# Performance work log

Measured on AMD Instinct MI355X. Metric: run time of the kernel, lower is better.

Reference implementation:

```python
import jax, jax.numpy as jnp
import numpy as np

DIM = 512
L = 4096
B, H, W = 8, 64, 64
EPS = 1e-06
BN_EPS = 1e-05


def setup_inputs() -> dict:
    key = jax.random.key(0)
    ks = jax.random.split(key, 16)
    s = 1.0 / np.sqrt(DIM)
    d = {
        'x': jax.random.normal(ks[0], (B, DIM, H, W), dtype=jnp.float32),
        'pos_emb': jax.random.normal(ks[1], (1, L, DIM), dtype=jnp.float32),
        'Wq': jax.random.uniform(ks[2], (DIM, DIM), jnp.float32, -s, s),
        'bq': jax.random.uniform(ks[3], (DIM,), jnp.float32, -s, s),
        'Wk': jax.random.uniform(ks[4], (DIM, DIM), jnp.float32, -s, s),
        'bk': jax.random.uniform(ks[5], (DIM,), jnp.float32, -s, s),
        'Wv': jax.random.uniform(ks[6], (DIM, DIM), jnp.float32, -s, s),
        'bv': jax.random.uniform(ks[7], (DIM,), jnp.float32, -s, s),
        'Wq1': jax.random.uniform(ks[8], (DIM, DIM), jnp.float32, -s, s),
        'bq1': jax.random.uniform(ks[9], (DIM,), jnp.float32, -s, s),
        'Wk1': jax.random.uniform(ks[10], (DIM, DIM), jnp.float32, -s, s),
        'bk1': jax.random.uniform(ks[11], (DIM,), jnp.float32, -s, s),
        'gamma': jax.random.normal(ks[12], (1,), jnp.float32) * 0.1,
        'bn_weight': jnp.ones((DIM,), jnp.float32),
        'bn_bias': jnp.zeros((DIM,), jnp.float32),
    }
    return d


def reference(x, pos_emb, Wq, bq, Wk, bk, Wv, bv, Wq1, bq1, Wk1, bk1, gamma, bn_weight, bn_bias):
    Bb, C, Hh, Ww = x.shape
    # [B,C,H,W] -> [B, L, C] tokens
    xs = x.transpose(0, 2, 3, 1).reshape(Bb, Hh * Ww, C) + pos_emb
    Q = jax.nn.relu(xs @ Wq.T + bq)   # kernel_fun = ReLU
    K = jax.nn.relu(xs @ Wk.T + bk)
    V = xs @ Wv.T + bv
    Q1 = xs @ Wq1.T + bq1
    K1 = xs @ Wk1.T + bk1
    # torch einsum 'blc,bcc,bl->blc' uses only diag(KV); compute it directly:
    # diagKV[b,c] = sum_l K[b,l,c] * V[b,l,c]
    diagKV = jnp.einsum('blc,blc->bc', K, V)
    Ksum = K.sum(axis=1)  # == K^T summed over last axis, [B,C]
    Z = 1.0 / jnp.einsum('blc,bc->bl', Q, Ksum + EPS)
    result = Q * diagKV[:, None, :] * Z[:, :, None]  # [B,L,C]
    # channel-softmax attention: softmax over last dim of Q1^T @ K1, [B,C,C]
    mid = jax.nn.softmax(jnp.einsum('blc,bld->bcd', Q1, K1), axis=-1)
    result = result @ mid  # [B,L,C]
    xs = xs + gamma * result
    y = xs.transpose(0, 2, 1).reshape(Bb, C, Hh, Ww)
    # BatchNorm2d in training mode (fresh module): batch stats, biased variance
    mean = y.mean(axis=(0, 2, 3))
    var = y.var(axis=(0, 2, 3))
    yn = (y - mean[None, :, None, None]) * jax.lax.rsqrt(var + BN_EPS)[None, :, None, None]
    yn = yn * bn_weight[None, :, None, None] + bn_bias[None, :, None, None]
    return jax.nn.relu(yn)
```

## Files before the change

### kernel.cpp

```cpp
#include <hip/hip_runtime.h>
#include <stdint.h>

typedef float f32x4 __attribute__((ext_vector_type(4)));
typedef short bf16x8 __attribute__((ext_vector_type(8)));

__device__ __forceinline__ float bf2f(unsigned short h){
  union { unsigned int u; float f; } v; v.u = ((unsigned int)h) << 16; return v.f;
}
__device__ __forceinline__ unsigned short f2bf(float f){
  union { float f; unsigned int u; } v; v.f = f;
  return (unsigned short)((v.u + 0x7fffu + ((v.u >> 16) & 1u)) >> 16);
}

typedef __attribute__((address_space(1))) const unsigned int ga_u32;
typedef __attribute__((address_space(3))) unsigned int ls_u32;
__device__ __forceinline__ void async_load16(const void* g, void* l){
  __builtin_amdgcn_global_load_lds((ga_u32*)g, (ls_u32*)l, 16, 0, 0);
}

#define CFENCE() asm volatile("" ::: "memory")
#define SB0() __builtin_amdgcn_sched_barrier(0)

__global__ __launch_bounds__(256) void k_prep_w(
    const float* __restrict__ w0, const float* __restrict__ w1,
// ... 1 lines not shown
    const float* __restrict__ w4, unsigned short* __restrict__ out)
{
  int i = blockIdx.x * 256 + threadIdx.x;
  const float* w = (blockIdx.y == 0) ? w0 : (blockIdx.y == 1) ? w1 :
                   (blockIdx.y == 2) ? w2 : (blockIdx.y == 3) ? w3 : w4;
  out[(size_t)blockIdx.y * 262144 + i] = f2bf(w[i]);
}
__global__ __launch_bounds__(256) void k_prep_b(
    const float* __restrict__ b0, const float* __restrict__ b1,
    const float* __restrict__ b2, const float* __restrict__ b3,
    const float* __restrict__ b4, float* __restrict__ out)
{
  int i = blockIdx.x * 256 + threadIdx.x;
  int s = i >> 9, r = i & 511;
  const float* b = (s == 0) ? b0 : (s == 1) ? b1 : (s == 2) ? b2 : (s == 3) ? b3 : b4;
  out[i] = b[r];
}

__global__ __launch_bounds__(256) void k_build_xs(
    const float* __restrict__ x, const float* __restrict__ pos,
    unsigned short* __restrict__ xsb)
{
  __shared__ float tile[64][65];
  const int lt = blockIdx.x, ct = blockIdx.y, b = blockIdx.z;
  const int t = threadIdx.x;
  const int rr = t >> 3, c8 = (t & 7) * 8;
  #pragma unroll
  for (int pass = 0; pass < 2; pass++){
    int r = rr + pass * 32;
    const float* src = x + ((size_t)b * 512 + ct*64 + r) * 4096 + lt*64 + c8;
    f32x4 v0 = *(const f32x4*)src;
    f32x4 v1 = *(const f32x4*)(src + 4);
    #pragma unroll
    for (int s = 0; s < 4; s++){ tile[r][c8+s] = v0[s]; tile[r][c8+4+s] = v1[s]; }
  }
  __syncthreads();
  #pragma unroll
  for (int pass = 0; pass < 2; pass++){
    int ll = rr + pass * 32;
    int gl = lt*64 + ll;
    const float* pp = pos + (size_t)gl * 512 + ct*64 + c8;
    bf16x8 hv;
    #pragma unroll
    for (int s = 0; s < 8; s++)
      hv[s] = (short)f2bf(tile[c8+s][ll] + pp[s]);
    *(bf16x8*)(xsb + ((size_t)b * 4096 + gl) * 512 + ct*64 + c8) = hv;
  }
}

__global__ __launch_bounds__(256) void k_transpose_scale(
    const unsigned short* __restrict__ in, const float* __restrict__ diag,
    unsigned short* __restrict__ out)
{
  __shared__ float tile[64][65];
  const int rt = blockIdx.x, ct = blockIdx.y, z = blockIdx.z;
  const unsigned short* src = in  + (size_t)z * 262144;
  unsigned short*       dst = out + (size_t)z * 262144;
  const int t = threadIdx.x;
  const int rr = t >> 3, c8 = (t & 7) * 8;
  #pragma unroll
  for (int pass = 0; pass < 2; pass++){
    int r = rr + pass * 32;
    bf16x8 v = *(const bf16x8*)(src + (size_t)(rt*64 + r) * 512 + ct*64 + c8);
    #pragma unroll
    for (int s = 0; s < 8; s++) tile[r][c8+s] = bf2f((unsigned short)v[s]);
  }
  __syncthreads();
  f32x4 dg0 = *(const f32x4*)(diag + z*512 + rt*64 + c8);
  f32x4 dg1 = *(const f32x4*)(diag + z*512 + rt*64 + c8 + 4);
  #pragma unroll
  for (int pass = 0; pass < 2; pass++){
    int c = rr + pass * 32;
    bf16x8 hv;
    #pragma unroll
    for (int s = 0; s < 4; s++) hv[s]   = (short)f2bf(tile[c8+s][c]   * dg0[s]);
    #pragma unroll
    for (int s = 0; s < 4; s++) hv[4+s] = (short)f2bf(tile[c8+4+s][c] * dg1[s]);
    *(bf16x8*)(dst + (size_t)(ct*64 + c) * 512 + rt*64 + c8) = hv;
  }
}

__global__ __launch_bounds__(256) void k_z(
    const unsigned short* __restrict__ Qb, const float* __restrict__ ksum,
    float* __restrict__ Z)
{
  const int row = blockIdx.x * 4 + (threadIdx.x >> 6);
  const int lane = threadIdx.x & 63;
  const int b = row >> 12;
  bf16x8 q = *(const bf16x8*)(Qb + (size_t)row * 512 + lane * 8);
  f32x4 k0 = *(const f32x4*)(ksum + b*512 + lane*8);
  f32x4 k1 = *(const f32x4*)(ksum + b*512 + lane*8 + 4);
  float den = 0.f;
  #pragma unroll
  for (int s = 0; s < 4; s++) den += bf2f((unsigned short)q[s])   * (k0[s] + 1e-6f);
  #pragma unroll
  for (int s = 0; s < 4; s++) den += bf2f((unsigned short)q[4+s]) * (k1[s] + 1e-6f);
  #pragma unroll
  for (int m = 1; m < 64; m <<= 1) den += __shfl_xor(den, m);
  if (lane == 0) Z[row] = 1.0f / den;
}

__global__ __launch_bounds__(64) void k_softmax(
    const float* __restrict__ S0, const float* __restrict__ S1,
    unsigned short* __restrict__ mid)
{
  const size_t row = blockIdx.x;
  const int lane = threadIdx.x;
  const float* p0 = S0 + row * 512 + lane * 8;
  const float* p1 = S1 + row * 512 + lane * 8;
  f32x4 v0 = *(const f32x4*)p0 + *(const f32x4*)p1;
  f32x4 v1 = *(const f32x4*)(p0 + 4) + *(const f32x4*)(p1 + 4);
  float mx = v0[0];
  #pragma unroll
  for (int s = 1; s < 4; s++) mx = fmaxf(mx, v0[s]);
  #pragma unroll
  for (int s = 0; s < 4; s++) mx = fmaxf(mx, v1[s]);
  #pragma unroll
  for (int m = 1; m < 64; m <<= 1) mx = fmaxf(mx, __shfl_xor(mx, m));
  float e[8]; float sum = 0.f;
  #pragma unroll
  for (int s = 0; s < 4; s++){ e[s]   = __expf(v0[s] - mx); sum += e[s]; }
  #pragma unroll
  for (int s = 0; s < 4; s++){ e[4+s] = __expf(v1[s] - mx); sum += e[4+s]; }
  #pragma unroll
  for (int m = 1; m < 64; m <<= 1) sum += __shfl_xor(sum, m);
  float inv = 1.0f / sum;
  bf16x8 hv;
  #pragma unroll
  for (int s = 0; s < 8; s++) hv[s] = (short)f2bf(e[s] * inv);
  *(bf16x8*)(mid + row * 512 + lane * 8) = hv;
}

#define GEMM_PRE()                                                            \
  const int tid = threadIdx.x;                                                \
  const int lane = tid & 63;                                                  \
  const int wave = tid >> 6;                                                  \
  const int wm = wave >> 1, wn = wave & 1;                                    \
  size_t aoff[4], boff[4]; int ldsq[4];                                       \
  _Pragma("unroll")                                                           \
  for (int i = 0; i < 4; i++){                                                \
    int qq = i*4 + wave;                                                      \
    int ch = qq*64 + lane;                                                    \
    int m  = ch >> 3, p = ch & 7;                                             \
    int lc = p ^ (m & 7);                                                     \
    aoff[i] = (size_t)(m0 + m) * K + lc*8;                                    \
    boff[i] = (size_t)(n0 + m) * K + lc*8;                                    \
    ldsq[i] = qq * 1024;                                                      \
  }                                                                           \
  f32x4 acc[4][4];                                                            \
  const f32x4 vzero = {0.f,0.f,0.f,0.f};                                      \
  _Pragma("unroll")                                                           \
  for (int i = 0; i < 4; i++)                                                 \
    _Pragma("unroll")                                                         \
    for (int j = 0; j < 4; j++) acc[i][j] = vzero;                            \
  int arow[4], brow[4];                                                       \
  _Pragma("unroll")                                                           \
  for (int f = 0; f < 4; f++){                                                \
    arow[f] = (wm*64 + f*16 + (lane & 15)) * 64;                              \
    brow[f] = (wn*64 + f*16 + (lane & 15)) * 64;                              \
  }                                                                           \
  const int kg = lane >> 4;                                                   \
  const int l7 = lane & 7;

#define GEMM_STAGE(buf, kt)                                                   \
  _Pragma("unroll")                                                           \
  for (int i = 0; i < 4; i++){                                                \
    async_load16(Ae + aoff[i] + (kt)*64, (char*)&smem[(buf)*8192] + ldsq[i]); \
    async_load16(Be + boff[i] + (kt)*64, (char*)&smem[16384 + (buf)*8192] + ldsq[i]); \
  }

#define GEMM_COMPUTE(buf)                                                     \
  _Pragma("unroll")                                                           \
  for (int ks = 0; ks < 2; ks++){                                             \
    bf16x8 a[4], b[4];                                                        \
    const int pa = (ks*4 + kg) ^ l7;                                          \
    _Pragma("unroll")                                                         \
    for (int f = 0; f < 4; f++){                                              \
      a[f] = *(const bf16x8*)&smem[(buf)*8192 + arow[f] + pa*8];              \
      b[f] = *(const bf16x8*)&smem[16384 + (buf)*8192 + brow[f] + pa*8];      \
    }                                                                         \
    _Pragma("unroll")                                                         \
    for (int i = 0; i < 4; i++)                                               \
      _Pragma("unroll")                                                       \
      for (int j = 0; j < 4; j++)                                             \
        acc[i][j] = __builtin_amdgcn_mfma_f32_16x16x32_bf16(a[i], b[j], acc[i][j], 0, 0, 0); \
  }

#define GEMM_KLOOP(nkt)                                                       \
  GEMM_STAGE(0, 0);                                                           \
  __syncthreads();                                                            \
  int cur = 0;                                                                \
  for (int kt = 0; kt < (nkt); kt++){                                         \
    if (kt + 1 < (nkt)) { GEMM_STAGE(cur ^ 1, kt + 1); }                      \
    GEMM_COMPUTE(cur);                                                        \
    __syncthreads();                                                          \
    cur ^= 1;                                                                 \
  }

__global__ __launch_bounds__(256) void gemm_mid(
    const unsigned short* __restrict__ A,
    const unsigned short* __restrict__ Bt,
    float* __restrict__ out0, float* __restrict__ out1)
{
  __shared__ unsigned short smem[32768];
  const int bid = blockIdx.x;
  const int wgid = (bid & 7) * 32 + (bid >> 3);
  const int part = wgid & 1;
  const int ntile = (wgid >> 1) & 3;
  const int mtile = (wgid >> 3) & 3;
  const int z = wgid >> 5;
  const int m0 = mtile * 128, n0 = ntile * 128;
  const int K = 4096;
  const unsigned short* Ae = A  + (size_t)z * 512 * 4096 + part * 2048;
  const unsigned short* Be = Bt + (size_t)z * 512 * 4096 + part * 2048;

  GEMM_PRE();
  GEMM_KLOOP(32);

  float* outf = part ? out1 : out0;
  const int lr = lane >> 4;
  const int lc16 = lane & 15;
  #pragma unroll
  for (int j = 0; j < 4; j++){
    int cidx = n0 + wn*64 + j*16 + lc16;
    #pragma unroll
    for (int i = 0; i < 4; i++){
      int r = m0 + wm*64 + i*16 + lr*4;
      #pragma unroll
      for (int q = 0; q < 4; q++)
        outf[(size_t)z * 262144 + (size_t)(r + q) * 512 + cidx] = acc[i][j][q];
    }
  }
}

#define G8_PRE(AE)                                                            \
  const int t = threadIdx.x;                                                  \
  const int lane = t & 63;                                                    \
  const int wave = t >> 6;                                                    \
  const int wm = wave >> 2, wn = wave & 3;                                    \
  const int l15 = lane & 15, kg = lane >> 4;                                  \
  const int lcw = ((t & 7) ^ ((t >> 3) & 7)) * 8;                             \
  const unsigned short* a_src = (AE) + (size_t)(m0 + (t >> 3)) * 512 + lcw;   \
  f32x4 acc[8][4];                                                            \
  const f32x4 vzero = {0.f,0.f,0.f,0.f};                                      \
  _Pragma("unroll")                                                           \
  for (int i = 0; i < 8; i++)                                                 \
    _Pragma("unroll")                                                         \
    for (int j = 0; j < 4; j++) acc[i][j] = vzero;                            \
  bf16x8 af[4][2], bf[4][2];

#define STAGE_A(D,H,TT) do{                                                   \
  async_load16(a_src + (H)*65536 + (TT)*64,                                   \
               (char*)smem + ((D)*16384 + (H)*8192 + t*8)*2);                 \
  async_load16(a_src + (H)*65536 + 32768 + (TT)*64,                           \
               (char*)smem + ((D)*16384 + (H)*8192 + 4096 + t*8)*2);          \
}while(0)

#define STAGE_B(D,H,TT) do{                                                   \
  async_load16(b_src + (H)*bhoff + (TT)*64,                                   \
               (char*)smem + (32768 + (D)*16384 + (H)*8192 + t*8)*2);         \
  async_load16(b_src + (H)*bhoff + 32768 + (TT)*64,                           \
               (char*)smem + (32768 + (D)*16384 + (H)*8192 + 4096 + t*8)*2);  \
}while(0)

#define READ_A(D, MH) do{                                                     \
  _Pragma("unroll")                                                           \
  for (int mfl = 0; mfl < 4; ++mfl){                                          \
    const int rl = ((MH)*4 + mfl)*16 + l15;                                   \
    _Pragma("unroll")                                                         \
    for (int ks = 0; ks < 2; ++ks){                                           \
      const int ck = (ks*4 + kg) ^ (rl & 7);                                  \
      af[mfl][ks] = *(const bf16x8*)&smem[(D)*16384 + wm*8192 + rl*64 + ck*8];\
    }                                                                         \
  }                                                                           \
}while(0)

#define READ_B(D, NP) do{                                                     \
  _Pragma("unroll")                                                           \
  for (int nfl = 0; nfl < 2; ++nfl){                                          \
    const int nf = (NP)*2 + nfl;                                              \
    const int rbl = (wn & 1)*64 + nf*16 + l15;                                \
    _Pragma("unroll")                                                         \
    for (int ks = 0; ks < 2; ++ks){                                           \
      const int ck = (ks*4 + kg) ^ (rbl & 7);                                 \
      bf[nf][ks] = *(const bf16x8*)&smem[32768 + (D)*16384 + (wn>>1)*8192 + rbl*64 + ck*8]; \
    }                                                                         \
  }                                                                           \
}while(0)

#define QUAD(MH, NP)                                                          \
  _Pragma("unroll")                                                           \
  for (int mfl = 0; mfl < 4; ++mfl)                                           \
    _Pragma("unroll")                                                         \
    for (int nfl = 0; nfl < 2; ++nfl)                                         \
      _Pragma("unroll")                                                       \
      for (int ks = 0; ks < 2; ++ks)                                          \
        acc[(MH)*4+mfl][(NP)*2+nfl] = __builtin_amdgcn_mfma_f32_16x16x32_bf16(\
            af[mfl][ks], bf[(NP)*2+nfl][ks], acc[(MH)*4+mfl][(NP)*2+nfl], 0,0,0);

#define PH_MID()  CFENCE(); __builtin_amdgcn_s_barrier();                     \
  __builtin_amdgcn_s_setprio(1); SB0()
#define PH_END()  SB0(); __builtin_amdgcn_s_setprio(0); CFENCE();             \
  __builtin_amdgcn_s_barrier(); CFENCE()
#define PH_END_VM4() SB0(); __builtin_amdgcn_s_setprio(0);                    \
  asm volatile("s_waitcnt vmcnt(4)" ::: "memory");                            \
  __builtin_amdgcn_s_barrier(); CFENCE()
#define PH_END_VM0() SB0(); __builtin_amdgcn_s_setprio(0);                    \
  asm volatile("s_waitcnt vmcnt(0)" ::: "memory");                            \
  __builtin_amdgcn_s_barrier(); CFENCE()

#define G8_KLOOP()                                                            \
  STAGE_A(0,0,0); STAGE_A(0,1,0); STAGE_B(0,0,0); STAGE_B(0,1,0);             \
  STAGE_B(1,0,1); STAGE_B(1,1,1);                                             \
  asm volatile("s_waitcnt vmcnt(4)" ::: "memory");                            \
  __builtin_amdgcn_s_barrier(); CFENCE();                                     \
  for (int it = 0; it < 3; ++it){                                             \
    const int t1 = 2*it + 1, t2 = 2*it + 2, t3 = 2*it + 3;                    \
    READ_A(0,0); READ_B(0,0); STAGE_A(1,0,t1);                                \
    PH_MID(); QUAD(0,0); PH_END();                                            \
    READ_B(0,1); STAGE_A(1,1,t1);                                             \
    PH_MID(); QUAD(0,1); PH_END();                                            \
    READ_A(0,1); STAGE_B(0,0,t2);                                             \
    PH_MID(); QUAD(1,0); PH_END();                                            \
    STAGE_A(0,0,t2);                                                          \
    PH_MID(); QUAD(1,1); PH_END_VM4();                                        \
    READ_A(1,0); READ_B(1,0); STAGE_A(0,1,t2);                                \
    PH_MID(); QUAD(0,0); PH_END();                                            \
    READ_B(1,1); STAGE_B(0,1,t2);                                             \
    PH_MID(); QUAD(0,1); PH_END();                                            \
    READ_A(1,1); STAGE_B(1,0,t3);                                             \
    PH_MID(); QUAD(1,0); PH_END();                                            \
    STAGE_B(1,1,t3);                                                          \
    PH_MID(); QUAD(1,1); PH_END_VM4();                                        \
  }                                                                           \
  {                           \
    READ_A(0,0); READ_B(0,0); STAGE_A(1,0,7);                                 \
    PH_MID(); QUAD(0,0); PH_END();                                            \
    READ_B(0,1); STAGE_A(1,1,7);                                              \
    PH_MID(); QUAD(0,1); PH_END();                                            \
    READ_A(0,1);                                                              \
    PH_MID(); QUAD(1,0); PH_END();                                            \
    PH_MID(); QUAD(1,1); PH_END_VM0();                                        \
    READ_A(1,0); READ_B(1,0);                                                 \
    PH_MID(); QUAD(0,0); PH_END();                                            \
    READ_B(1,1);                                                              \
    PH_MID(); QUAD(0,1); PH_END();                                            \
    READ_A(1,1);                                                              \
    PH_MID(); QUAD(1,0); PH_END();                                            \
    PH_MID(); QUAD(1,1); PH_END();                                            \
  }

__global__ __launch_bounds__(512, 2) void gemm8_proj(
    const unsigned short* __restrict__ A,
    const unsigned short* __restrict__ W,
    const float* __restrict__ bias5,
    unsigned short* __restrict__ Qb,
    unsigned short* __restrict__ Q1T, unsigned short* __restrict__ K1T,
    float* __restrict__ diag, float* __restrict__ ksum)
{
  __shared__ unsigned short smem[65536];
  const int bid = blockIdx.x;
  const int wgid = (bid & 7) * 160 + (bid >> 3);
  const int mtile = wgid / 10;
  const int nslot = wgid % 10;
  const int m0 = mtile * 256;

  int mode, wsel = 0, nbase = 0, p = 0;
  if (nslot < 2)      { mode = 0; wsel = 0; nbase = nslot * 256; }
  else if (nslot < 6) { mode = 1; p = nslot - 2; }
  else if (nslot < 8) { mode = 2; wsel = 3; nbase = (nslot - 6) * 256; }
  else                { mode = 3; wsel = 4; nbase = (nslot - 8) * 256; }

  G8_PRE(A);
  const unsigned short* b_src; int bhoff;
  if (mode == 1){
    b_src = W + 262144 + (size_t)(p*128 + (t >> 3)) * 512 + lcw;
    bhoff = 262144;
  } else {
    b_src = W + (size_t)wsel * 262144 + (size_t)(nbase + (t >> 3)) * 512 + lcw;
    bhoff = 65536;
  }

  G8_KLOOP();

  if (mode == 0){
    __syncthreads();
    #pragma unroll
    for (int nf = 0; nf < 4; nf++){
      int cl = wn*64 + nf*16 + l15;
      float bb = bias5[nbase + cl];
      #pragma unroll
      for (int mf = 0; mf < 8; mf++){
        int rbase = wm*128 + mf*16 + kg*4;
        #pragma unroll
        for (int q = 0; q < 4; q++){
          float v = acc[mf][nf][q] + bb;
          v = v > 0.f ? v : 0.f;
          int rl = rbase + q;
          smem[rl*256 + (cl ^ (((rl >> 2) & 3) << 4))] = f2bf(v);
        }
      }
    }
    __syncthreads();
    const int c0 = (t & 31) * 8;
    #pragma unroll
    for (int rep = 0; rep < 16; rep++){
      int rl = rep*16 + (t >> 5);
      bf16x8 v = *(const bf16x8*)&smem[rl*256 + (c0 ^ (((rl >> 2) & 3) << 4))];
      *(bf16x8*)(Qb + (size_t)(m0 + rl) * 512 + nbase + c0) = v;
    }
  } else if (mode == 1){
    const int b = mtile >> 4;
    __syncthreads();
    if (wn < 2){
      #pragma unroll
      for (int nf = 0; nf < 4; nf++){
        int cl = (wn & 1)*64 + nf*16 + l15;
        float bb = bias5[512 + p*128 + cl];
        float ks_ = 0.f;
        #pragma unroll
        for (int mf = 0; mf < 8; mf++){
          int rbase = wm*128 + mf*16 + kg*4;
          #pragma unroll
          for (int q = 0; q < 4; q++){
            float v = acc[mf][nf][q] + bb;
            v = v > 0.f ? v : 0.f;
            unsigned short h = f2bf(v);
            int r = rbase + q;
            smem[r*128 + (cl ^ (((r >> 2) & 7) << 4))] = h;
            ks_ += bf2f(h);
          }
        }
        ks_ += __shfl_xor(ks_, 16);
        ks_ += __shfl_xor(ks_, 32);
        if (kg == 0) atomicAdd(&ksum[b*512 + p*128 + cl], ks_);
      }
    }
    __syncthreads();
    if (wn >= 2){
      #pragma unroll
      for (int nf = 0; nf < 4; nf++){
        int cl = (wn & 1)*64 + nf*16 + l15;
        float bb = bias5[1024 + p*128 + cl];
        float dv = 0.f;
        #pragma unroll
        for (int mf = 0; mf < 8; mf++){
          int rbase = wm*128 + mf*16 + kg*4;
          #pragma unroll
          for (int q = 0; q < 4; q++){
            int r = rbase + q;
            float kf = bf2f(smem[r*128 + (cl ^ (((r >> 2) & 7) << 4))]);
            float vf = bf2f(f2bf(acc[mf][nf][q] + bb));
            dv += kf * vf;
          }
        }
        dv += __shfl_xor(dv, 16);
        dv += __shfl_xor(dv, 32);
        if (kg == 0) atomicAdd(&diag[b*512 + p*128 + cl], dv);
      }
    }
  } else {
    unsigned short* o = (mode == 2) ? Q1T : K1T;
    const int b = mtile >> 4;
    const int l0 = (mtile & 15) * 256;
    __syncthreads();
    #pragma unroll
    for (int nf = 0; nf < 4; nf++){
      int cl_ = wn*64 + nf*16 + l15;
      float bb = bias5[wsel*512 + nbase + cl_];
      #pragma unroll
      for (int mf = 0; mf < 8; mf++){
        #pragma unroll
        for (int q = 0; q < 4; q++){
          int ll = wm*128 + mf*16 + kg*4 + q;
          int sw = ((ll >> 3) ^ (cl_ & 7)) * 8 + (ll & 7);
          smem[cl_*256 + sw] = f2bf(acc[mf][nf][q] + bb);
        }
      }
    }
    __syncthreads();
    #pragma unroll
    for (int rep = 0; rep < 16; rep++){
      int c = rep*16 + (t >> 5);
      int lch = t & 31;
      bf16x8 v = *(const bf16x8*)&smem[c*256 + (lch ^ (c & 7))*8];
      *(bf16x8*)(o + ((size_t)b*512 + nbase + c)*4096 + l0 + lch*8) = v;
    }
  }
}

__global__ __launch_bounds__(512, 2) void gemm8_res(
    const unsigned short* __restrict__ A,
    const unsigned short* __restrict__ Bt,
    const float* __restrict__ Zp,
    unsigned short* __restrict__ outh,
    const float* __restrict__ gamma_p,
    float* __restrict__ bnS, float* __restrict__ bnQ)
{
  __shared__ unsigned short smem[65536];
  __shared__ float zbuf[256];
  const int bid = blockIdx.x;
  const int wgid = (bid & 7) * 32 + (bid >> 3);
  const int mtile = wgid >> 1;
  const int ntile = wgid & 1;
  const int m0 = mtile * 256;
  const int nc0 = ntile * 256;

  G8_PRE(A);
  const unsigned short* b_src =
      Bt + (size_t)(mtile >> 4) * 262144 + (size_t)(nc0 + (t >> 3)) * 512 + lcw;
  const int bhoff = 65536;

  G8_KLOOP();

  const float g = gamma_p[0];
  __syncthreads();
  if (t < 256) zbuf[t] = Zp[m0 + t];
  __syncthreads();
  #pragma unroll
  for (int nf = 0; nf < 4; nf++){
    int cl = wn*64 + nf*16 + l15;
    #pragma unroll
    for (int mf = 0; mf < 8; mf++){
      int rbase = wm*128 + mf*16 + kg*4;
      #pragma unroll
      for (int q = 0; q < 4; q++){
        int rl = rbase + q;
        smem[rl*256 + (cl ^ (((rl >> 2) & 3) << 4))] =
            f2bf(g * zbuf[rl] * acc[mf][nf][q]);
      }
    }
  }
  __syncthreads();
  float sc[8] = {0.f,0.f,0.f,0.f,0.f,0.f,0.f,0.f};
  float sq[8] = {0.f,0.f,0.f,0.f,0.f,0.f,0.f,0.f};
  const int c0 = (t & 31) * 8;
  #pragma unroll
  for (int rep = 0; rep < 16; rep++){
    int rl = rep*16 + (t >> 5);
    bf16x8 ga = *(const bf16x8*)&smem[rl*256 + (c0 ^ (((rl >> 2) & 3) << 4))];
    size_t gidx = (size_t)(m0 + rl) * 512 + nc0 + c0;
    bf16x8 xv = *(const bf16x8*)(outh + gidx);
    bf16x8 yv;
    #pragma unroll
    for (int j = 0; j < 8; j++){
      float y = bf2f((unsigned short)xv[j]) + bf2f((unsigned short)ga[j]);
      yv[j] = (short)f2bf(y);
      sc[j] += y; sq[j] += y * y;
    }
    *(bf16x8*)(outh + gidx) = yv;
  }
  __syncthreads();
// ... 69 lines not shown
  const float* Wq   = (const float*)d_in[2];
  const float* bq   = (const float*)d_in[3];
  const float* Wk   = (const float*)d_in[4];
  const float* bk   = (const float*)d_in[5];
  const float* Wv   = (const float*)d_in[6];
  const float* bv   = (const float*)d_in[7];
  const float* Wq1  = (const float*)d_in[8];
  const float* bq1  = (const float*)d_in[9];
  const float* Wk1  = (const float*)d_in[10];
  const float* bk1  = (const float*)d_in[11];
  const float* gam  = (const float*)d_in[12];
  const float* bnw  = (const float*)d_in[13];
  const float* bnb  = (const float*)d_in[14];
  float* out = (float*)d_out;
  char* ws = (char*)d_ws;

  const size_t MB = 1ull << 20;
  const size_t OFF_XSB  = 0;
  const size_t OFF_QB   = 32*MB;
  const size_t OFF_Q1T  = 64*MB;
  const size_t OFF_K1T  = 96*MB;
  const size_t OFF_SF0  = 128*MB;
  const size_t OFF_SF1  = 136*MB;
  const size_t OFF_MIDB = 144*MB;
  const size_t OFF_MIDT = 148*MB;
  const size_t OFF_WBF  = 152*MB;
  const size_t OFF_B5   = 155*MB;
  const size_t OFF_Z    = 156*MB;
  const size_t OFF_DIAG = 157*MB;
  const size_t OFF_KSUM = OFF_DIAG + 16384;
  const size_t OFF_BNS  = OFF_KSUM + 16384;
  const size_t OFF_BNQ  = OFF_BNS + 2048;
  const size_t WS_NEED  = OFF_BNQ + 2048;
  if (ws_size < WS_NEED) return;

  unsigned short* xsb  = (unsigned short*)(ws + OFF_XSB);
  unsigned short* Qb   = (unsigned short*)(ws + OFF_QB);
  unsigned short* Q1T  = (unsigned short*)(ws + OFF_Q1T);
  unsigned short* K1T  = (unsigned short*)(ws + OFF_K1T);
  float*          Sf0  = (float*)(ws + OFF_SF0);
  float*          Sf1  = (float*)(ws + OFF_SF1);
  unsigned short* midb = (unsigned short*)(ws + OFF_MIDB);
  unsigned short* midT = (unsigned short*)(ws + OFF_MIDT);
  unsigned short* wbf  = (unsigned short*)(ws + OFF_WBF);
  float* bias5 = (float*)(ws + OFF_B5);
  float* Zp   = (float*)(ws + OFF_Z);
  float* diag = (float*)(ws + OFF_DIAG);
  float* ksum = (float*)(ws + OFF_KSUM);
  float* bnS  = (float*)(ws + OFF_BNS);
  float* bnQ  = (float*)(ws + OFF_BNQ);

  hipMemsetAsync(ws + OFF_DIAG, 0, 16384 + 16384 + 2048 + 2048, stream);

  k_prep_w  <<<dim3(1024, 5), 256, 0, stream>>>(Wq, Wk, Wv, Wq1, Wk1, wbf);
  k_prep_b  <<<dim3(10),      256, 0, stream>>>(bq, bk, bv, bq1, bk1, bias5);
  k_build_xs<<<dim3(64, 8, 8),256, 0, stream>>>(x, pos, xsb);

  gemm8_proj<<<dim3(1280), 512, 0, stream>>>(xsb, wbf, bias5, Qb, Q1T, K1T, diag, ksum);

  k_z<<<dim3(8192), 256, 0, stream>>>(Qb, ksum, Zp);

  gemm_mid<<<dim3(256), 256, 0, stream>>>(Q1T, K1T, Sf0, Sf1);

  k_softmax<<<dim3(4096), 64, 0, stream>>>(Sf0, Sf1, midb);

  k_transpose_scale<<<dim3(8, 8, 8), 256, 0, stream>>>(midb, diag, midT);

  gemm8_res<<<dim3(256), 512, 0, stream>>>(Qb, midT, Zp, xsb, gam, bnS, bnQ);

  k_bn_finalize<<<dim3(64, 8, 8), 256, 0, stream>>>(xsb, bnS, bnQ, bnw, bnb, out);
}
```

Before: 234.8 us.

## Fuse softmax with transpose-scale, fold Z into residual GEMM, retile projection GEMM

Merges the channel softmax, diag scaling and transpose into one kernel, and computes the Z normaliser inside the residual GEMM from ksum, which removes the k_z and k_transpose_scale launches and their intermediate buffers. The projection GEMM is replaced by a 128x128-tile, 256-thread kernel that runs the K and V projections back to back in one block, so K·V and Ksum come from registers. k_build_xs now loops over the batch to reuse pos_emb loads. The trade-off is smaller GEMM tiles with less reuse per block, and a softmax kernel with only 64 blocks and limited parallelism.

```diff
diff --git a/kernel.cpp b/kernel.cpp
--- a/kernel.cpp
+++ b/kernel.cpp
@@ -47,113 +47,85 @@
     unsigned short* __restrict__ xsb)
 {
   __shared__ float tile[64][65];
-  const int lt = blockIdx.x, ct = blockIdx.y, b = blockIdx.z;
+  const int lt = blockIdx.x, ct = blockIdx.y;
   const int t = threadIdx.x;
   const int rr = t >> 3, c8 = (t & 7) * 8;
+  float pr[16];
   #pragma unroll
   for (int pass = 0; pass < 2; pass++){
-    int r = rr + pass * 32;
-    const float* src = x + ((size_t)b * 512 + ct*64 + r) * 4096 + lt*64 + c8;
-    f32x4 v0 = *(const f32x4*)src;
-    f32x4 v1 = *(const f32x4*)(src + 4);
-    #pragma unroll
-    for (int s = 0; s < 4; s++){ tile[r][c8+s] = v0[s]; tile[r][c8+4+s] = v1[s]; }
+    int gl = lt*64 + rr + pass*32;
+    f32x4 p0 = *(const f32x4*)(pos + (size_t)gl * 512 + ct*64 + c8);
+    f32x4 p1 = *(const f32x4*)(pos + (size_t)gl * 512 + ct*64 + c8 + 4);
+    #pragma unroll
+    for (int s = 0; s < 4; s++){ pr[pass*8+s] = p0[s]; pr[pass*8+4+s] = p1[s]; }
+  }
+  for (int b = 0; b < 8; b++){
+    #pragma unroll
+    for (int pass = 0; pass < 2; pass++){
+      int r = rr + pass * 32;
+      const float* src = x + ((size_t)b * 512 + ct*64 + r) * 4096 + lt*64 + c8;
+      f32x4 v0 = *(const f32x4*)src;
+      f32x4 v1 = *(const f32x4*)(src + 4);
+      #pragma unroll
+      for (int s = 0; s < 4; s++){ tile[r][c8+s] = v0[s]; tile[r][c8+4+s] = v1[s]; }
+    }
+    __syncthreads();
+    #pragma unroll
+    for (int pass = 0; pass < 2; pass++){
+      int ll = rr + pass * 32;
+      int gl = lt*64 + ll;
+      bf16x8 hv;
+      #pragma unroll
+      for (int s = 0; s < 8; s++)
+        hv[s] = (short)f2bf(tile[c8+s][ll] + pr[pass*8+s]);
+      *(bf16x8*)(xsb + ((size_t)b * 4096 + gl) * 512 + ct*64 + c8) = hv;
+    }
+    __syncthreads();
+  }
+}
+
+__global__ __launch_bounds__(256) void k_softmax_t(
+    const float* __restrict__ S0, const float* __restrict__ S1,
+    const float* __restrict__ diag, unsigned short* __restrict__ midT)
+{
+  __shared__ unsigned short tr[64 * 514];
+  const int it = blockIdx.x, z = blockIdx.y;
+  const int t = threadIdx.x;
+  const int lane = t & 63, w = t >> 6;
+  for (int rr = 0; rr < 16; rr++){
+    int i = rr*4 + w;
+    size_t rowo = (size_t)z * 262144 + (size_t)(it*64 + i) * 512 + lane*8;
+    const float* p0 = S0 + rowo;
+    const float* p1 = S1 + rowo;
+    f32x4 v0 = *(const f32x4*)p0 + *(const f32x4*)p1;
+    f32x4 v1 = *(const f32x4*)(p0 + 4) + *(const f32x4*)(p1 + 4);
+    float mx = v0[0];
+    #pragma unroll
+    for (int s = 1; s < 4; s++) mx = fmaxf(mx, v0[s]);
+    #pragma unroll
+    for (int s = 0; s < 4; s++) mx = fmaxf(mx, v1[s]);
+    #pragma unroll
+    for (int m = 1; m < 64; m <<= 1) mx = fmaxf(mx, __shfl_xor(mx, m));
+    float e[8]; float sum = 0.f;
+    #pragma unroll
+    for (int s = 0; s < 4; s++){ e[s]   = __expf(v0[s] - mx); sum += e[s]; }
+    #pragma unroll
+    for (int s = 0; s < 4; s++){ e[4+s] = __expf(v1[s] - mx); sum += e[4+s]; }
+    #pragma unroll
+    for (int m = 1; m < 64; m <<= 1) sum += __shfl_xor(sum, m);
+    float sc = diag[z*512 + it*64 + i] / sum;
+    #pragma unroll
+    for (int s = 0; s < 8; s++) tr[i*514 + lane*8 + s] = f2bf(e[s] * sc);
   }
   __syncthreads();
-  #pragma unroll
-  for (int pass = 0; pass < 2; pass++){
-    int ll = rr + pass * 32;
-    int gl = lt*64 + ll;
-    const float* pp = pos + (size_t)gl * 512 + ct*64 + c8;
+  for (int ps = 0; ps < 16; ps++){
+    int j = ps*32 + (t >> 3);
+    int i0 = (t & 7) * 8;
     bf16x8 hv;
     #pragma unroll
-    for (int s = 0; s < 8; s++)
-      hv[s] = (short)f2bf(tile[c8+s][ll] + pp[s]);
-    *(bf16x8*)(xsb + ((size_t)b * 4096 + gl) * 512 + ct*64 + c8) = hv;
-  }
-}
-
-__global__ __launch_bounds__(256) void k_transpose_scale(
-    const unsigned short* __restrict__ in, const float* __restrict__ diag,
-    unsigned short* __restrict__ out)
-{
-  __shared__ float tile[64][65];
-  const int rt = blockIdx.x, ct = blockIdx.y, z = blockIdx.z;
-  const unsigned short* src = in  + (size_t)z * 262144;
-  unsigned short*       dst = out + (size_t)z * 262144;
-  const int t = threadIdx.x;
-  const int rr = t >> 3, c8 = (t & 7) * 8;
-  #pragma unroll
-  for (int pass = 0; pass < 2; pass++){
-    int r = rr + pass * 32;
-    bf16x8 v = *(const bf16x8*)(src + (size_t)(rt*64 + r) * 512 + ct*64 + c8);
-    #pragma unroll
-    for (int s = 0; s < 8; s++) tile[r][c8+s] = bf2f((unsigned short)v[s]);
-  }
-  __syncthreads();
-  f32x4 dg0 = *(const f32x4*)(diag + z*512 + rt*64 + c8);
-  f32x4 dg1 = *(const f32x4*)(diag + z*512 + rt*64 + c8 + 4);
-  #pragma unroll
-  for (int pass = 0; pass < 2; pass++){
-    int c = rr + pass * 32;
-    bf16x8 hv;
-    #pragma unroll
-    for (int s = 0; s < 4; s++) hv[s]   = (short)f2bf(tile[c8+s][c]   * dg0[s]);
-    #pragma unroll
-    for (int s = 0; s < 4; s++) hv[4+s] = (short)f2bf(tile[c8+4+s][c] * dg1[s]);
-    *(bf16x8*)(dst + (size_t)(ct*64 + c) * 512 + rt*64 + c8) = hv;
-  }
-}
-
-__global__ __launch_bounds__(256) void k_z(
-    const unsigned short* __restrict__ Qb, const float* __restrict__ ksum,
-    float* __restrict__ Z)
-{
-  const int row = blockIdx.x * 4 + (threadIdx.x >> 6);
-  const int lane = threadIdx.x & 63;
-  const int b = row >> 12;
-  bf16x8 q = *(const bf16x8*)(Qb + (size_t)row * 512 + lane * 8);
-  f32x4 k0 = *(const f32x4*)(ksum + b*512 + lane*8);
-  f32x4 k1 = *(const f32x4*)(ksum + b*512 + lane*8 + 4);
-  float den = 0.f;
-  #pragma unroll
-  for (int s = 0; s < 4; s++) den += bf2f((unsigned short)q[s])   * (k0[s] + 1e-6f);
-  #pragma unroll
-  for (int s = 0; s < 4; s++) den += bf2f((unsigned short)q[4+s]) * (k1[s] + 1e-6f);
-  #pragma unroll
-  for (int m = 1; m < 64; m <<= 1) den += __shfl_xor(den, m);
-  if (lane == 0) Z[row] = 1.0f / den;
-}
-
-__global__ __launch_bounds__(64) void k_softmax(
-    const float* __restrict__ S0, const float* __restrict__ S1,
-    unsigned short* __restrict__ mid)
-{
-  const size_t row = blockIdx.x;
-  const int lane = threadIdx.x;
-  const float* p0 = S0 + row * 512 + lane * 8;
-  const float* p1 = S1 + row * 512 + lane * 8;
-  f32x4 v0 = *(const f32x4*)p0 + *(const f32x4*)p1;
-  f32x4 v1 = *(const f32x4*)(p0 + 4) + *(const f32x4*)(p1 + 4);
-  float mx = v0[0];
-  #pragma unroll
-  for (int s = 1; s < 4; s++) mx = fmaxf(mx, v0[s]);
-  #pragma unroll
-  for (int s = 0; s < 4; s++) mx = fmaxf(mx, v1[s]);
-  #pragma unroll
-  for (int m = 1; m < 64; m <<= 1) mx = fmaxf(mx, __shfl_xor(mx, m));
-  float e[8]; float sum = 0.f;
-  #pragma unroll
-  for (int s = 0; s < 4; s++){ e[s]   = __expf(v0[s] - mx); sum += e[s]; }
-  #pragma unroll
-  for (int s = 0; s < 4; s++){ e[4+s] = __expf(v1[s] - mx); sum += e[4+s]; }
-  #pragma unroll
-  for (int m = 1; m < 64; m <<= 1) sum += __shfl_xor(sum, m);
-  float inv = 1.0f / sum;
-  bf16x8 hv;
-  #pragma unroll
-  for (int s = 0; s < 8; s++) hv[s] = (short)f2bf(e[s] * inv);
-  *(bf16x8*)(mid + row * 512 + lane * 8) = hv;
+    for (int s = 0; s < 8; s++) hv[s] = (short)tr[(i0+s)*514 + j];
+    *(bf16x8*)(midT + ((size_t)z*512 + j)*512 + it*64 + i0) = hv;
+  }
 }
 
 #define GEMM_PRE()                                                            \
@@ -169,7 +141,7 @@
     int m  = ch >> 3, p = ch & 7;                                             \
     int lc = p ^ (m & 7);                                                     \
     aoff[i] = (size_t)(m0 + m) * K + lc*8;                                    \
-    boff[i] = (size_t)(n0 + m) * K + lc*8;                                    \
+    boff[i] = (size_t)m * K + lc*8;                                           \
     ldsq[i] = qq * 1024;                                                      \
   }                                                                           \
   f32x4 acc[4][4];                                                            \
@@ -185,16 +157,17 @@
     brow[f] = (wn*64 + f*16 + (lane & 15)) * 64;                              \
   }                                                                           \
   const int kg = lane >> 4;                                                   \
-  const int l7 = lane & 7;
-
-#define GEMM_STAGE(buf, kt)                                                   \
+  const int l7 = lane & 7;                                                    \
+  const int l15 = lane & 15;
+
+#define GEMM_STAGE2(buf, kt, BB)                                              \
   _Pragma("unroll")                                                           \
   for (int i = 0; i < 4; i++){                                                \
     async_load16(Ae + aoff[i] + (kt)*64, (char*)&smem[(buf)*8192] + ldsq[i]); \
-    async_load16(Be + boff[i] + (kt)*64, (char*)&smem[16384 + (buf)*8192] + ldsq[i]); \
-  }
-
-#define GEMM_COMPUTE(buf)                                                     \
+    async_load16((BB) + boff[i] + (kt)*64, (char*)&smem[16384 + (buf)*8192] + ldsq[i]); \
+  }
+
+#define GEMM_COMPUTE2(buf, ACC)                                               \
   _Pragma("unroll")                                                           \
   for (int ks = 0; ks < 2; ks++){                                             \
     bf16x8 a[4], b[4];                                                        \
@@ -208,19 +181,19 @@
     for (int i = 0; i < 4; i++)                                               \
       _Pragma("unroll")                                                       \
       for (int j = 0; j < 4; j++)                                             \
-        acc[i][j] = __builtin_amdgcn_mfma_f32_16x16x32_bf16(a[i], b[j], acc[i][j], 0, 0, 0); \
-  }
-
-#define GEMM_KLOOP(nkt)                                                       \
-  GEMM_STAGE(0, 0);                                                           \
+        (ACC)[i][j] = __builtin_amdgcn_mfma_f32_16x16x32_bf16(a[i], b[j], (ACC)[i][j], 0, 0, 0); \
+  }
+
+#define GEMM_KLOOP2(nkt, BB)                                                  \
+  GEMM_STAGE2(0, 0, BB);                                                      \
   __syncthreads();                                                            \
-  int cur = 0;                                                                \
-  for (int kt = 0; kt < (nkt); kt++){                                         \
-    if (kt + 1 < (nkt)) { GEMM_STAGE(cur ^ 1, kt + 1); }                      \
-    GEMM_COMPUTE(cur);                                                        \
-    __syncthreads();                                                          \
-    cur ^= 1;                                                                 \
-  }
+  { int cur = 0;                                                              \
+    for (int kt = 0; kt < (nkt); kt++){                                       \
+      if (kt + 1 < (nkt)) { GEMM_STAGE2(cur ^ 1, kt + 1, BB); }               \
+      GEMM_COMPUTE2(cur, acc);                                                \
+      __syncthreads();                                                        \
+      cur ^= 1;                                                               \
+    } }
 
 __global__ __launch_bounds__(256) void gemm_mid(
     const unsigned short* __restrict__ A,
@@ -236,24 +209,165 @@
   const int z = wgid >> 5;
   const int m0 = mtile * 128, n0 = ntile * 128;
   const int K = 4096;
-  const unsigned short* Ae = A  + (size_t)z * 512 * 4096 + part * 2048;
-  const unsigned short* Be = Bt + (size_t)z * 512 * 4096 + part * 2048;
+  const unsigned short* Ae = A  + (size_t)z * 2097152 + part * 2048;
+  const unsigned short* Be = Bt + (size_t)z * 2097152 + part * 2048 + (size_t)n0 * 4096;
 
   GEMM_PRE();
-  GEMM_KLOOP(32);
+  GEMM_KLOOP2(32, Be);
 
   float* outf = part ? out1 : out0;
-  const int lr = lane >> 4;
-  const int lc16 = lane & 15;
   #pragma unroll
   for (int j = 0; j < 4; j++){
-    int cidx = n0 + wn*64 + j*16 + lc16;
+    int cidx = n0 + wn*64 + j*16 + l15;
     #pragma unroll
     for (int i = 0; i < 4; i++){
-      int r = m0 + wm*64 + i*16 + lr*4;
+      int r = m0 + wm*64 + i*16 + kg*4;
       #pragma unroll
       for (int q = 0; q < 4; q++)
         outf[(size_t)z * 262144 + (size_t)(r + q) * 512 + cidx] = acc[i][j][q];
+    }
+  }
+}
+
+__global__ __launch_bounds__(256, 2) void gemm_proj2(
+    const unsigned short* __restrict__ A,
+    const unsigned short* __restrict__ W,
+    const float* __restrict__ bias5,
+    unsigned short* __restrict__ Qb,
+    unsigned short* __restrict__ Q1T, unsigned short* __restrict__ K1T,
+    float* __restrict__ diag, float* __restrict__ ksum)
+{
+  __shared__ unsigned short smem[32768];
+  const int bid = blockIdx.x;
+  const int wgid = (bid & 7) * 512 + (bid >> 3);
+  const int mtile = wgid >> 4;
+  const int unit  = wgid & 15;
+  const int m0 = mtile * 128;
+  const int K = 512;
+  const unsigned short* Ae = A;
+
+  int mode, cb;
+  const unsigned short* BeK; const unsigned short* BeV = W;
+  if (unit < 4)      { mode = 0; cb = unit*128;      BeK = W + (size_t)cb * 512; }
+  else if (unit < 8) { mode = 1; cb = (unit-4)*128;  BeK = W + 262144 + (size_t)cb * 512;
+                                                     BeV = W + 524288 + (size_t)cb * 512; }
+  else if (unit < 12){ mode = 2; cb = (unit-8)*128;  BeK = W + 786432 + (size_t)cb * 512; }
+  else               { mode = 3; cb = (unit-12)*128; BeK = W + 1048576 + (size_t)cb * 512; }
+
+  GEMM_PRE();
+
+  if (mode == 1){
+    const int bz = mtile >> 5;
+    GEMM_STAGE2(0, 0, BeK);
+    __syncthreads();
+    int cur = 0;
+    for (int kt = 0; kt < 8; kt++){
+      if (kt < 7) { GEMM_STAGE2(cur ^ 1, kt + 1, BeK); }
+      else        { GEMM_STAGE2(cur ^ 1, 0, BeV); }
+      GEMM_COMPUTE2(cur, acc);
+      __syncthreads();
+      cur ^= 1;
+    }
+    GEMM_STAGE2(cur ^ 1, 1, BeV);
+    unsigned int kpk[4][4][2];
+    #pragma unroll
+    for (int j = 0; j < 4; j++){
+      const int cj = cb + wn*64 + j*16 + l15;
+      const float bb = bias5[512 + cj];
+      float ks_ = 0.f;
+      #pragma unroll
+      for (int i = 0; i < 4; i++){
+        #pragma unroll
+        for (int h = 0; h < 2; h++){
+          float v0 = acc[i][j][2*h]   + bb; v0 = v0 > 0.f ? v0 : 0.f;
+          float v1 = acc[i][j][2*h+1] + bb; v1 = v1 > 0.f ? v1 : 0.f;
+          unsigned short h0 = f2bf(v0), h1 = f2bf(v1);
+          kpk[i][j][h] = (unsigned)h0 | ((unsigned)h1 << 16);
+          ks_ += bf2f(h0) + bf2f(h1);
+        }
+        acc[i][j] = vzero;
+      }
+      ks_ += __shfl_xor(ks_, 16);
+      ks_ += __shfl_xor(ks_, 32);
+      if (lane < 16) atomicAdd(&ksum[bz*512 + cj], ks_);
+    }
+    for (int kt = 0; kt < 8; kt++){
+      if (kt >= 1 && kt < 7) { GEMM_STAGE2(cur ^ 1, kt + 1, BeV); }
+      GEMM_COMPUTE2(cur, acc);
+      __syncthreads();
+      cur ^= 1;
+    }
+    #pragma unroll
+    for (int j = 0; j < 4; j++){
+      const int cj = cb + wn*64 + j*16 + l15;
+      const float bb = bias5[1024 + cj];
+      float dv = 0.f;
+      #pragma unroll
+      for (int i = 0; i < 4; i++){
+        #pragma unroll
+        for (int h = 0; h < 2; h++){
+          float v0 = bf2f(f2bf(acc[i][j][2*h]   + bb));
+          float v1 = bf2f(f2bf(acc[i][j][2*h+1] + bb));
+          dv += bf2f((unsigned short)(kpk[i][j][h] & 0xffffu)) * v0
+              + bf2f((unsigned short)(kpk[i][j][h] >> 16))     * v1;
+        }
+      }
+      dv += __shfl_xor(dv, 16);
+      dv += __shfl_xor(dv, 32);
+      if (lane < 16) atomicAdd(&diag[bz*512 + cj], dv);
+    }
+    return;
+  }
+
+  GEMM_KLOOP2(8, BeK);
+
+  if (mode == 0){
+    #pragma unroll
+    for (int j = 0; j < 4; j++){
+      const int cl = wn*64 + j*16 + l15;
+      const float bb = bias5[cb + cl];
+      #pragma unroll
+      for (int i = 0; i < 4; i++){
+        const int rb = wm*64 + i*16 + kg*4;
+        #pragma unroll
+        for (int q = 0; q < 4; q++){
+          float v = acc[i][j][q] + bb; v = v > 0.f ? v : 0.f;
+          smem[(rb + q)*136 + cl] = f2bf(v);
+        }
+      }
+    }
+    __syncthreads();
+    #pragma unroll
+    for (int rep = 0; rep < 8; rep++){
+      const int rl = rep*16 + (tid >> 4);
+      const int c0 = (tid & 15) * 8;
+      bf16x8 v = *(const bf16x8*)&smem[rl*136 + c0];
+      *(bf16x8*)(Qb + (size_t)(m0 + rl) * 512 + cb + c0) = v;
+    }
+  } else {
+    unsigned short* o = (mode == 2) ? Q1T : K1T;
+    const int bz = mtile >> 5;
+    const int l0 = (mtile & 31) * 128;
+    const int bco = (mode == 2) ? 1536 : 2048;
+    #pragma unroll
+    for (int j = 0; j < 4; j++){
+      const int cl = wn*64 + j*16 + l15;
+      const float bb = bias5[bco + cb + cl];
+      #pragma unroll
+      for (int i = 0; i < 4; i++){
+        const int lb = wm*64 + i*16 + kg*4;
+        #pragma unroll
+        for (int q = 0; q < 4; q++)
+          smem[cl*136 + lb + q] = f2bf(acc[i][j][q] + bb);
+      }
+    }
+    __syncthreads();
+    #pragma unroll
+    for (int rep = 0; rep < 8; rep++){
+      const int cl = rep*16 + (tid >> 4);
+      const int lch = tid & 15;
+      bf16x8 v = *(const bf16x8*)&smem[cl*136 + lch*8];
+      *(bf16x8*)(o + ((size_t)bz*512 + cb + cl)*4096 + l0 + lch*8) = v;
     }
   }
 }
@@ -264,6 +378,7 @@
   const int wave = t >> 6;                                                    \
   const int wm = wave >> 2, wn = wave & 3;                                    \
   const int l15 = lane & 15, kg = lane >> 4;                                  \
+  const int l7 = lane & 7;                                                    \
   const int lcw = ((t & 7) ^ ((t >> 3) & 7)) * 8;                             \
   const unsigned short* a_src = (AE) + (size_t)(m0 + (t >> 3)) * 512 + lcw;   \
   f32x4 acc[8][4];                                                            \
@@ -282,9 +397,9 @@
 }while(0)
 
 #define STAGE_B(D,H,TT) do{                                                   \
-  async_load16(b_src + (H)*bhoff + (TT)*64,                                   \
+  async_load16(b_src + (H)*65536 + (TT)*64,                                   \
                (char*)smem + (32768 + (D)*16384 + (H)*8192 + t*8)*2);         \
-  async_load16(b_src + (H)*bhoff + 32768 + (TT)*64,                           \
+  async_load16(b_src + (H)*65536 + 32768 + (TT)*64,                           \
                (char*)smem + (32768 + (D)*16384 + (H)*8192 + 4096 + t*8)*2);  \
 }while(0)
 
@@ -313,6 +428,21 @@
   }                                                                           \
 }while(0)
 
+#define ZDOT(KT, MH) do{ if ((wave & 3) == 0){                                \
+  _Pragma("unroll")                                                           \
+  for (int ks = 0; ks < 2; ++ks){                                             \
+    const int ck = (ks*4 + kg) ^ l7;                                          \
+    f32x4 ka = *(const f32x4*)&kse[(KT)*64 + ck*8];                           \
+    f32x4 kb = *(const f32x4*)&kse[(KT)*64 + ck*8 + 4];                       \
+    _Pragma("unroll")                                                         \
+    for (int mfl = 0; mfl < 4; ++mfl){                                        \
+      _Pragma("unroll")                                                       \
+      for (int jj = 0; jj < 4; ++jj)                                          \
+        zacc[(MH)*4+mfl] += bf2f((unsigned short)af[mfl][ks][jj])   * ka[jj]  \
+                          + bf2f((unsigned short)af[mfl][ks][4+jj]) * kb[jj]; \
+    }                                                                         \
+  } } }while(0)
+
 #define QUAD(MH, NP)                                                          \
   _Pragma("unroll")                                                           \
   for (int mfl = 0; mfl < 4; ++mfl)                                           \
@@ -334,213 +464,83 @@
   asm volatile("s_waitcnt vmcnt(0)" ::: "memory");                            \
   __builtin_amdgcn_s_barrier(); CFENCE()
 
-#define G8_KLOOP()                                                            \
+#define G8_KLOOP_Z()                                                          \
   STAGE_A(0,0,0); STAGE_A(0,1,0); STAGE_B(0,0,0); STAGE_B(0,1,0);             \
   STAGE_B(1,0,1); STAGE_B(1,1,1);                                             \
   asm volatile("s_waitcnt vmcnt(4)" ::: "memory");                            \
   __builtin_amdgcn_s_barrier(); CFENCE();                                     \
   for (int it = 0; it < 3; ++it){                                             \
     const int t1 = 2*it + 1, t2 = 2*it + 2, t3 = 2*it + 3;                    \
-    READ_A(0,0); READ_B(0,0); STAGE_A(1,0,t1);                                \
+    READ_A(0,0); ZDOT(2*it,0); READ_B(0,0); STAGE_A(1,0,t1);                  \
     PH_MID(); QUAD(0,0); PH_END();                                            \
     READ_B(0,1); STAGE_A(1,1,t1);                                             \
     PH_MID(); QUAD(0,1); PH_END();                                            \
-    READ_A(0,1); STAGE_B(0,0,t2);                                             \
+    READ_A(0,1); ZDOT(2*it,1); STAGE_B(0,0,t2);                               \
     PH_MID(); QUAD(1,0); PH_END();                                            \
     STAGE_A(0,0,t2);                                                          \
     PH_MID(); QUAD(1,1); PH_END_VM4();                                        \
-    READ_A(1,0); READ_B(1,0); STAGE_A(0,1,t2);                                \
+    READ_A(1,0); ZDOT(2*it+1,0); READ_B(1,0); STAGE_A(0,1,t2);                \
     PH_MID(); QUAD(0,0); PH_END();                                            \
     READ_B(1,1); STAGE_B(0,1,t2);                                             \
     PH_MID(); QUAD(0,1); PH_END();                                            \
-    READ_A(1,1); STAGE_B(1,0,t3);                                             \
+    READ_A(1,1); ZDOT(2*it+1,1); STAGE_B(1,0,t3);                             \
     PH_MID(); QUAD(1,0); PH_END();                                            \
     STAGE_B(1,1,t3);                                                          \
     PH_MID(); QUAD(1,1); PH_END_VM4();                                        \
   }                                                                           \
-  {                           \
-    READ_A(0,0); READ_B(0,0); STAGE_A(1,0,7);                                 \
+  { READ_A(0,0); ZDOT(6,0); READ_B(0,0); STAGE_A(1,0,7);                      \
     PH_MID(); QUAD(0,0); PH_END();                                            \
     READ_B(0,1); STAGE_A(1,1,7);                                              \
     PH_MID(); QUAD(0,1); PH_END();                                            \
-    READ_A(0,1);                                                              \
+    READ_A(0,1); ZDOT(6,1);                                                   \
     PH_MID(); QUAD(1,0); PH_END();                                            \
     PH_MID(); QUAD(1,1); PH_END_VM0();                                        \
-    READ_A(1,0); READ_B(1,0);                                                 \
+    READ_A(1,0); ZDOT(7,0); READ_B(1,0);                                      \
     PH_MID(); QUAD(0,0); PH_END();                                            \
     READ_B(1,1);                                                              \
     PH_MID(); QUAD(0,1); PH_END();                                            \
-    READ_A(1,1);                                                              \
+    READ_A(1,1); ZDOT(7,1);                                                   \
     PH_MID(); QUAD(1,0); PH_END();                                            \
-    PH_MID(); QUAD(1,1); PH_END();                                            \
-  }
-
-__global__ __launch_bounds__(512, 2) void gemm8_proj(
-    const unsigned short* __restrict__ A,
-    const unsigned short* __restrict__ W,
-    const float* __restrict__ bias5,
-    unsigned short* __restrict__ Qb,
-    unsigned short* __restrict__ Q1T, unsigned short* __restrict__ K1T,
-    float* __restrict__ diag, float* __restrict__ ksum)
-{
-  __shared__ unsigned short smem[65536];
-  const int bid = blockIdx.x;
-  const int wgid = (bid & 7) * 160 + (bid >> 3);
-  const int mtile = wgid / 10;
-  const int nslot = wgid % 10;
-  const int m0 = mtile * 256;
-
-  int mode, wsel = 0, nbase = 0, p = 0;
-  if (nslot < 2)      { mode = 0; wsel = 0; nbase = nslot * 256; }
-  else if (nslot < 6) { mode = 1; p = nslot - 2; }
-  else if (nslot < 8) { mode = 2; wsel = 3; nbase = (nslot - 6) * 256; }
-  else                { mode = 3; wsel = 4; nbase = (nslot - 8) * 256; }
-
-  G8_PRE(A);
-  const unsigned short* b_src; int bhoff;
-  if (mode == 1){
-    b_src = W + 262144 + (size_t)(p*128 + (t >> 3)) * 512 + lcw;
-    bhoff = 262144;
-  } else {
-    b_src = W + (size_t)wsel * 262144 + (size_t)(nbase + (t >> 3)) * 512 + lcw;
-    bhoff = 65536;
-  }
-
-  G8_KLOOP();
-
-  if (mode == 0){
-    __syncthreads();
-    #pragma unroll
-    for (int nf = 0; nf < 4; nf++){
-      int cl = wn*64 + nf*16 + l15;
-      float bb = bias5[nbase + cl];
-      #pragma unroll
-      for (int mf = 0; mf < 8; mf++){
-        int rbase = wm*128 + mf*16 + kg*4;
-        #pragma unroll
-        for (int q = 0; q < 4; q++){
-          float v = acc[mf][nf][q] + bb;
-          v = v > 0.f ? v : 0.f;
-          int rl = rbase + q;
-          smem[rl*256 + (cl ^ (((rl >> 2) & 3) << 4))] = f2bf(v);
-        }
-      }
-    }
-    __syncthreads();
-    const int c0 = (t & 31) * 8;
-    #pragma unroll
-    for (int rep = 0; rep < 16; rep++){
-      int rl = rep*16 + (t >> 5);
-      bf16x8 v = *(const bf16x8*)&smem[rl*256 + (c0 ^ (((rl >> 2) & 3) << 4))];
-      *(bf16x8*)(Qb + (size_t)(m0 + rl) * 512 + nbase + c0) = v;
-    }
-  } else if (mode == 1){
-    const int b = mtile >> 4;
-    __syncthreads();
-    if (wn < 2){
-      #pragma unroll
-      for (int nf = 0; nf < 4; nf++){
-        int cl = (wn & 1)*64 + nf*16 + l15;
-        float bb = bias5[512 + p*128 + cl];
-        float ks_ = 0.f;
-        #pragma unroll
-        for (int mf = 0; mf < 8; mf++){
-          int rbase = wm*128 + mf*16 + kg*4;
-          #pragma unroll
-          for (int q = 0; q < 4; q++){
-            float v = acc[mf][nf][q] + bb;
-            v = v > 0.f ? v : 0.f;
-            unsigned short h = f2bf(v);
-            int r = rbase + q;
-            smem[r*128 + (cl ^ (((r >> 2) & 7) << 4))] = h;
-            ks_ += bf2f(h);
-          }
-        }
-        ks_ += __shfl_xor(ks_, 16);
-        ks_ += __shfl_xor(ks_, 32);
-        if (kg == 0) atomicAdd(&ksum[b*512 + p*128 + cl], ks_);
-      }
-    }
-    __syncthreads();
-    if (wn >= 2){
-      #pragma unroll
-      for (int nf = 0; nf < 4; nf++){
-        int cl = (wn & 1)*64 + nf*16 + l15;
-        float bb = bias5[1024 + p*128 + cl];
-        float dv = 0.f;
-        #pragma unroll
-        for (int mf = 0; mf < 8; mf++){
-          int rbase = wm*128 + mf*16 + kg*4;
-          #pragma unroll
-          for (int q = 0; q < 4; q++){
-            int r = rbase + q;
-            float kf = bf2f(smem[r*128 + (cl ^ (((r >> 2) & 7) << 4))]);
-            float vf = bf2f(f2bf(acc[mf][nf][q] + bb));
-            dv += kf * vf;
-          }
-        }
-        dv += __shfl_xor(dv, 16);
-        dv += __shfl_xor(dv, 32);
-        if (kg == 0) atomicAdd(&diag[b*512 + p*128 + cl], dv);
-      }
-    }
-  } else {
-    unsigned short* o = (mode == 2) ? Q1T : K1T;
-    const int b = mtile >> 4;
-    const int l0 = (mtile & 15) * 256;
-    __syncthreads();
-    #pragma unroll
-    for (int nf = 0; nf < 4; nf++){
-      int cl_ = wn*64 + nf*16 + l15;
-      float bb = bias5[wsel*512 + nbase + cl_];
-      #pragma unroll
-      for (int mf = 0; mf < 8; mf++){
-        #pragma unroll
-        for (int q = 0; q < 4; q++){
-          int ll = wm*128 + mf*16 + kg*4 + q;
-          int sw = ((ll >> 3) ^ (cl_ & 7)) * 8 + (ll & 7);
-          smem[cl_*256 + sw] = f2bf(acc[mf][nf][q] + bb);
-        }
-      }
-    }
-    __syncthreads();
-    #pragma unroll
-    for (int rep = 0; rep < 16; rep++){
-      int c = rep*16 + (t >> 5);
-      int lch = t & 31;
-      bf16x8 v = *(const bf16x8*)&smem[c*256 + (lch ^ (c & 7))*8];
-      *(bf16x8*)(o + ((size_t)b*512 + nbase + c)*4096 + l0 + lch*8) = v;
-    }
-  }
-}
+    PH_MID(); QUAD(1,1); PH_END(); }
 
 __global__ __launch_bounds__(512, 2) void gemm8_res(
     const unsigned short* __restrict__ A,
     const unsigned short* __restrict__ Bt,
-    const float* __restrict__ Zp,
+    const float* __restrict__ ksum,
     unsigned short* __restrict__ outh,
     const float* __restrict__ gamma_p,
     float* __restrict__ bnS, float* __restrict__ bnQ)
 {
   __shared__ unsigned short smem[65536];
-  __shared__ float zbuf[256];
+  __shared__ float kse[512];
+  __shared__ float zlds[256];
   const int bid = blockIdx.x;
   const int wgid = (bid & 7) * 32 + (bid >> 3);
   const int mtile = wgid >> 1;
   const int ntile = wgid & 1;
   const int m0 = mtile * 256;
   const int nc0 = ntile * 256;
+  const int bz = mtile >> 4;
 
   G8_PRE(A);
   const unsigned short* b_src =
-      Bt + (size_t)(mtile >> 4) * 262144 + (size_t)(nc0 + (t >> 3)) * 512 + lcw;
-  const int bhoff = 65536;
-
-  G8_KLOOP();
-
+      Bt + (size_t)bz * 262144 + (size_t)(nc0 + (t >> 3)) * 512 + lcw;
+  float zacc[8] = {0.f,0.f,0.f,0.f,0.f,0.f,0.f,0.f};
+  kse[t & 511] = ksum[bz*512 + (t & 511)] + 1e-6f;
+  __syncthreads();
+
+  G8_KLOOP_Z();
+
+  if ((wave & 3) == 0){
+    #pragma unroll
+    for (int r8 = 0; r8 < 8; r8++){
+      float zz = zacc[r8];
+      zz += __shfl_xor(zz, 16);
+      zz += __shfl_xor(zz, 32);
+      if (kg == 0) zlds[wm*128 + r8*16 + l15] = 1.0f / zz;
+    }
+  }
   const float g = gamma_p[0];
-  __syncthreads();
-  if (t < 256) zbuf[t] = Zp[m0 + t];
   __syncthreads();
   #pragma unroll
   for (int nf = 0; nf < 4; nf++){
@@ -552,7 +552,7 @@
       for (int q = 0; q < 4; q++){
         int rl = rbase + q;
         smem[rl*256 + (cl ^ (((rl >> 2) & 3) << 4))] =
-            f2bf(g * zbuf[rl] * acc[mf][nf][q]);
+            f2bf(g * zlds[rl] * acc[mf][nf][q]);
       }
     }
   }
@@ -668,12 +668,10 @@
   const size_t OFF_K1T  = 96*MB;
   const size_t OFF_SF0  = 128*MB;
   const size_t OFF_SF1  = 136*MB;
-  const size_t OFF_MIDB = 144*MB;
-  const size_t OFF_MIDT = 148*MB;
-  const size_t OFF_WBF  = 152*MB;
-  const size_t OFF_B5   = 155*MB;
-  const size_t OFF_Z    = 156*MB;
-  const size_t OFF_DIAG = 157*MB;
+  const size_t OFF_MIDT = 144*MB;
+  const size_t OFF_WBF  = 148*MB;
+  const size_t OFF_B5   = 151*MB;
+  const size_t OFF_DIAG = 152*MB;
   const size_t OFF_KSUM = OFF_DIAG + 16384;
   const size_t OFF_BNS  = OFF_KSUM + 16384;
   const size_t OFF_BNQ  = OFF_BNS + 2048;
@@ -686,11 +684,9 @@
   unsigned short* K1T  = (unsigned short*)(ws + OFF_K1T);
   float*          Sf0  = (float*)(ws + OFF_SF0);
   float*          Sf1  = (float*)(ws + OFF_SF1);
-  unsigned short* midb = (unsigned short*)(ws + OFF_MIDB);
   unsigned short* midT = (unsigned short*)(ws + OFF_MIDT);
   unsigned short* wbf  = (unsigned short*)(ws + OFF_WBF);
   float* bias5 = (float*)(ws + OFF_B5);
-  float* Zp   = (float*)(ws + OFF_Z);
   float* diag = (float*)(ws + OFF_DIAG);
   float* ksum = (float*)(ws + OFF_KSUM);
   float* bnS  = (float*)(ws + OFF_BNS);
@@ -700,19 +696,15 @@
 
   k_prep_w  <<<dim3(1024, 5), 256, 0, stream>>>(Wq, Wk, Wv, Wq1, Wk1, wbf);
   k_prep_b  <<<dim3(10),      256, 0, stream>>>(bq, bk, bv, bq1, bk1, bias5);
-  k_build_xs<<<dim3(64, 8, 8),256, 0, stream>>>(x, pos, xsb);
-
-  gemm8_proj<<<dim3(1280), 512, 0, stream>>>(xsb, wbf, bias5, Qb, Q1T, K1T, diag, ksum);
-
-  k_z<<<dim3(8192), 256, 0, stream>>>(Qb, ksum, Zp);
+  k_build_xs<<<dim3(64, 8),   256, 0, stream>>>(x, pos, xsb);
+
+  gemm_proj2<<<dim3(4096), 256, 0, stream>>>(xsb, wbf, bias5, Qb, Q1T, K1T, diag, ksum);
 
   gemm_mid<<<dim3(256), 256, 0, stream>>>(Q1T, K1T, Sf0, Sf1);
 
-  k_softmax<<<dim3(4096), 64, 0, stream>>>(Sf0, Sf1, midb);
-
-  k_transpose_scale<<<dim3(8, 8, 8), 256, 0, stream>>>(midb, diag, midT);
-
-  gemm8_res<<<dim3(256), 512, 0, stream>>>(Qb, midT, Zp, xsb, gam, bnS, bnQ);
+  k_softmax_t<<<dim3(8, 8), 256, 0, stream>>>(Sf0, Sf1, diag, midT);
+
+  gemm8_res<<<dim3(256), 512, 0, stream>>>(Qb, midT, ksum, xsb, gam, bnS, bnQ);
 
   k_bn_finalize<<<dim3(64, 8, 8), 256, 0, stream>>>(xsb, bnS, bnQ, bnw, bnb, out);
 }
```

Result: slower. 257.7 us (+9.8%).
